# Performance work log

Measured on AMD Instinct MI355X. Metric: run time of the kernel, lower is better.

## Reference

```python
import math
import jax, jax.numpy as jnp
import numpy as np

B, S, HID = 1, 2048, 2880
H, HKV, D = 64, 8, 64
G = H // HKV  # num_key_value_groups = 8


def setup_inputs() -> dict:
    key = jax.random.key(0)
    ks = jax.random.split(key, 10)
    sd = 1.0 / math.sqrt(HID)
    hidden_states = jax.random.normal(ks[0], (B, S, HID), dtype=jnp.float32)
    # causal additive mask [B, 1, S, S]
    causal = jnp.tril(jnp.ones((S, S), dtype=bool))
    attention_mask = jnp.where(causal, 0.0, -1e9).astype(jnp.float32)[None, None]
    Wq = jax.random.normal(ks[1], (H * D, HID), dtype=jnp.float32) * sd
    bq = jax.random.normal(ks[2], (H * D,), dtype=jnp.float32) * 0.01
    Wk = jax.random.normal(ks[3], (HKV * D, HID), dtype=jnp.float32) * sd
    bk = jax.random.normal(ks[4], (HKV * D,), dtype=jnp.float32) * 0.01
    Wv = jax.random.normal(ks[5], (HKV * D, HID), dtype=jnp.float32) * sd
    bv = jax.random.normal(ks[6], (HKV * D,), dtype=jnp.float32) * 0.01
    Wo = jax.random.normal(ks[7], (HID, H * D), dtype=jnp.float32) * (1.0 / math.sqrt(H * D))
    bo = jax.random.normal(ks[8], (HID,), dtype=jnp.float32) * 0.01
    return {"hidden_states": hidden_states, "attention_mask": attention_mask,
            "Wq": Wq, "bq": bq, "Wk": Wk, "bk": bk, "Wv": Wv, "bv": bv,
            "Wo": Wo, "bo": bo}


def reference(hidden_states, attention_mask, Wq, bq, Wk, bk, Wv, bv, Wo, bo):
    b, s, _ = hidden_states.shape
    # projections
    q = hidden_states @ Wq.T + bq  # [b, s, H*D]
    k = hidden_states @ Wk.T + bk  # [b, s, HKV*D]
    v = hidden_states @ Wv.T + bv
    # torch q head index h maps to kv head h // G, so split H -> (HKV, G)
    q = q.reshape(b, s, HKV, G, D).transpose(0, 2, 3, 1, 4)   # [b, kv, g, s, d]
    k = k.reshape(b, s, HKV, D).transpose(0, 2, 1, 3)         # [b, kv, s, d]
    v = v.reshape(b, s, HKV, D).transpose(0, 2, 1, 3)
    # grouped-query attention without materializing repeated KV (same math as repeat_interleave)
    scores = jnp.einsum('bkgsd,bktd->bkgst', q, k) / math.sqrt(D)
    scores = scores + attention_mask[:, :, None]              # broadcast [b,1,1,s,t]
    attn = jax.nn.softmax(scores.astype(jnp.float32), axis=-1).astype(q.dtype)
    out = jnp.einsum('bkgst,bktd->bkgsd', attn, v)            # [b, kv, g, s, d]
    out = out.transpose(0, 3, 1, 2, 4).reshape(b, s, H * D)
    return out @ Wo.T + bo
```

## Files before the change

kernel.cpp:

```cpp
#include <hip/hip_runtime.h>
#include <hip/hip_bf16.h>
#include <cmath>

typedef __hip_bfloat16 bf16;
typedef __bf16 bf16x8 __attribute__((ext_vector_type(8)));
typedef float floatx4 __attribute__((ext_vector_type(4)));

__device__ inline floatx4 mfma16(bf16x8 a, bf16x8 b, floatx4 c) {
  return __builtin_amdgcn_mfma_f32_16x16x32_bf16(a, b, c, 0, 0, 0);
}

__device__ inline void async_ld16(const void* g, void* l) {
  __builtin_amdgcn_global_load_lds((const __attribute__((address_space(1))) void*)g,
                                   (__attribute__((address_space(3))) void*)l,
                                   16, 0, 0);
}

__device__ inline uint4 pack8(float4 a, float4 b) {
  union { uint4 u; bf16 h[8]; } t;
  t.h[0] = __float2bfloat16(a.x); t.h[1] = __float2bfloat16(a.y);
  t.h[2] = __float2bfloat16(a.z); t.h[3] = __float2bfloat16(a.w);
  t.h[4] = __float2bfloat16(b.x); t.h[5] = __float2bfloat16(b.y);
  t.h[6] = __float2bfloat16(b.z); t.h[7] = __float2bfloat16(b.w);
  return t.u;
}

__device__ inline void cvt_region(const float* __restrict__ s, bf16* __restrict__ d, int i) {
  const float4 a = ((const float4*)s)[2 * i];
  const float4 b = ((const float4*)s)[2 * i + 1];
  ((uint4*)d)[i] = pack8(a, b);
}

__global__ __launch_bounds__(256)
void cvt_all(const float* __restrict__ X,  const float* __restrict__ Wq,
             const float* __restrict__ Wk, const float* __restrict__ Wv,
             const float* __restrict__ Wo, bf16* __restrict__ Xb,
             bf16* __restrict__ Wall, bf16* __restrict__ Wob) {
  const int blk = blockIdx.x;
  const int tid = threadIdx.x;
  if (blk < 2880) {
    cvt_region(X, Xb, blk * 256 + tid);
  } else if (blk < 8640) {
    cvt_region(Wq, Wall, (blk - 2880) * 256 + tid);
  } else if (blk < 9360) {
    cvt_region(Wk, Wall + (size_t)4096 * 2880, (blk - 8640) * 256 + tid);
  } else if (blk < 10080) {
    cvt_region(Wv, Wall + (size_t)4608 * 2880, (blk - 9360) * 256 + tid);
  } else {
    cvt_region(Wo, Wob, (blk - 10080) * 256 + tid);
  }
}

#define QSCALE 0.1803368801111601f

template <int OUT_MODE>
__global__ __launch_bounds__(256)
void gemm_bt_db(const bf16* __restrict__ A, const bf16* __restrict__ B,
                const float* __restrict__ b0, const float* __restrict__ b1,
                const float* __restrict__ b2, void* __restrict__ Cp,
                void* __restrict__ Cqp, void* __restrict__ Ctp,
                int M, int N, int K, float qmul) {
  __shared__ __align__(16) bf16 sA[2][128 * 32];
  __shared__ __align__(16) bf16 sB[2][128 * 32];
  const int tid  = threadIdx.x;
  const int wave = tid >> 6;
  const int lane = tid & 63;
  const int quad = lane >> 4;
  const int l15  = lane & 15;

  const int nwg = gridDim.x * gridDim.y;
  const int lin = blockIdx.y * gridDim.x + blockIdx.x;
  const int L   = (lin & 7) * (nwg >> 3) + (lin >> 3);
  const int bm  = (L / gridDim.x) * 128;
  const int bn  = (L % gridDim.x) * 128;

  const int wm = (wave & 1) * 64;
  const int wn = (wave >> 1) * 64;

  floatx4 acc[4][4] = {};

  const int g0 = tid, g1 = tid + 256;
  const int arow0 = bm + (g0 >> 2), acol0 = (g0 & 3) * 8;
  const int arow1 = bm + (g1 >> 2), acol1 = (g1 & 3) * 8;
  int brow0 = bn + (g0 >> 2); if (brow0 >= N) brow0 = N - 1;
  int brow1 = bn + (g1 >> 2); if (brow1 >= N) brow1 = N - 1;

  const int nk = K >> 5;
  async_ld16(A + (size_t)arow0 * K + acol0, &sA[0][wave * 512]);
  async_ld16(A + (size_t)arow1 * K + acol1, &sA[0][2048 + wave * 512]);
  async_ld16(B + (size_t)brow0 * K + acol0, &sB[0][wave * 512]);
  async_ld16(B + (size_t)brow1 * K + acol1, &sB[0][2048 + wave * 512]);

  for (int kt = 0; kt < nk; ++kt) {
    __syncthreads();
    if (kt + 1 < nk) {
      const int k0 = (kt + 1) << 5;
      const int nb = (kt + 1) & 1;
      async_ld16(A + (size_t)arow0 * K + k0 + acol0, &sA[nb][wave * 512]);
      async_ld16(A + (size_t)arow1 * K + k0 + acol1, &sA[nb][2048 + wave * 512]);
      async_ld16(B + (size_t)brow0 * K + k0 + acol0, &sB[nb][wave * 512]);
      async_ld16(B + (size_t)brow1 * K + k0 + acol1, &sB[nb][2048 + wave * 512]);
    }
    const bf16* a = sA[kt & 1];
    const bf16* b = sB[kt & 1];

    bf16x8 aF[4], bF[4];
#pragma unroll
    for (int mi = 0; mi < 4; ++mi)
      aF[mi] = *(const bf16x8*)(a + (wm + mi * 16 + l15) * 32 + quad * 8);
#pragma unroll
    for (int ni = 0; ni < 4; ++ni)
      bF[ni] = *(const bf16x8*)(b + (wn + ni * 16 + l15) * 32 + quad * 8);
#pragma unroll
    for (int mi = 0; mi < 4; ++mi)
#pragma unroll
      for (int ni = 0; ni < 4; ++ni)
        acc[mi][ni] = mfma16(aF[mi], bF[ni], acc[mi][ni]);
  }

#pragma unroll
  for (int ni = 0; ni < 4; ++ni) {
    const int col = bn + wn + ni * 16 + l15;
    if (col >= N) continue;
    float bv;
    if (OUT_MODE == 4)
      bv = (col < 4096) ? b0[col] : (col < 4608 ? b1[col - 4096] : b2[col - 4608]);
    else
      bv = b0[col];
#pragma unroll
    for (int mi = 0; mi < 4; ++mi) {
      const int row = bm + wm + mi * 16 + quad * 4;
#pragma unroll
      for (int r = 0; r < 4; ++r) {
        const float val = acc[mi][ni][r] + bv;
        if (OUT_MODE == 1) {
          ((float*)Cp)[(size_t)(row + r) * N + col] = val;
        } else {
          if (col < 4096)      ((bf16*)Cp)[(size_t)(row + r) * 4096 + col] = __float2bfloat16(val * qmul);
          else if (col < 4608) ((bf16*)Cqp)[(size_t)(row + r) * 512 + (col - 4096)] = __float2bfloat16(val);
          else                 ((bf16*)Ctp)[(size_t)(col - 4608) * M + row + r] = __float2bfloat16(val);
        }
      }
    }
  }
}

template <int A_BF, int B_BF, int OUT_MODE>
__global__ __launch_bounds__(256)
void gemm_bt_bias(const void* __restrict__ Ap, const void* __restrict__ Bp,
                  const float* __restrict__ bias, void* __restrict__ Cp,
                  void* __restrict__ Cqp, void* __restrict__ Ctp,
                  int M, int N, int K, float qmul) {
  __shared__ __align__(16) bf16 sA[128 * 32];
  __shared__ __align__(16) bf16 sB[128 * 32];
  const int tid  = threadIdx.x;
  const int wave = tid >> 6;
  const int lane = tid & 63;
  const int quad = lane >> 4;
  const int l15  = lane & 15;
  const int bm = blockIdx.y * 128;
  const int bn = blockIdx.x * 128;
  const int wm = (wave & 1) * 64;
  const int wn = (wave >> 1) * 64;

  floatx4 acc[4][4] = {};

  const int g0 = tid, g1 = tid + 256;
  const int arow0 = bm + (g0 >> 2), acol0 = (g0 & 3) * 8;
  const int arow1 = bm + (g1 >> 2), acol1 = (g1 & 3) * 8;
  int brow0 = bn + (g0 >> 2); if (brow0 >= N) brow0 = N - 1;
  int brow1 = bn + (g1 >> 2); if (brow1 >= N) brow1 = N - 1;

  for (int k0 = 0; k0 < K; k0 += 32) {
    __syncthreads();
    if (A_BF) {
      const bf16* A = (const bf16*)Ap;
      async_ld16(A + (size_t)arow0 * K + k0 + acol0, sA + wave * 512);
      async_ld16(A + (size_t)arow1 * K + k0 + acol1, sA + 2048 + wave * 512);
    } else {
      const float* A = (const float*)Ap;
      const float* p0 = A + (size_t)arow0 * K + k0 + acol0;
      const float* p1 = A + (size_t)arow1 * K + k0 + acol1;
      *(uint4*)(sA + tid * 8)        = pack8(*(const float4*)p0, *(const float4*)(p0 + 4));
      *(uint4*)(sA + 2048 + tid * 8) = pack8(*(const float4*)p1, *(const float4*)(p1 + 4));
    }
    if (B_BF) {
      const bf16* B = (const bf16*)Bp;
      async_ld16(B + (size_t)brow0 * K + k0 + acol0, sB + wave * 512);
      async_ld16(B + (size_t)brow1 * K + k0 + acol1, sB + 2048 + wave * 512);
    } else {
      const float* B = (const float*)Bp;
      const float* p0 = B + (size_t)brow0 * K + k0 + acol0;
      const float* p1 = B + (size_t)brow1 * K + k0 + acol1;
      *(uint4*)(sB + tid * 8)        = pack8(*(const float4*)p0, *(const float4*)(p0 + 4));
      *(uint4*)(sB + 2048 + tid * 8) = pack8(*(const float4*)p1, *(const float4*)(p1 + 4));
    }
    __syncthreads();

    bf16x8 aF[4], bF[4];
#pragma unroll
    for (int mi = 0; mi < 4; ++mi)
      aF[mi] = *(const bf16x8*)(sA + (wm + mi * 16 + l15) * 32 + quad * 8);
#pragma unroll
    for (int ni = 0; ni < 4; ++ni)
      bF[ni] = *(const bf16x8*)(sB + (wn + ni * 16 + l15) * 32 + quad * 8);
#pragma unroll
    for (int mi = 0; mi < 4; ++mi)
#pragma unroll
      for (int ni = 0; ni < 4; ++ni)
        acc[mi][ni] = mfma16(aF[mi], bF[ni], acc[mi][ni]);
  }

#pragma unroll
  for (int ni = 0; ni < 4; ++ni) {
    const int col = bn + wn + ni * 16 + l15;
    if (col >= N) continue;
    const float bv = bias[col];
#pragma unroll
    for (int mi = 0; mi < 4; ++mi) {
      const int row = bm + wm + mi * 16 + quad * 4;
#pragma unroll
      for (int r = 0; r < 4; ++r) {
        const float val = acc[mi][ni][r] + bv;
        if (OUT_MODE == 0) {
          ((bf16*)Cp)[(size_t)(row + r) * N + col] = __float2bfloat16(val * qmul);
        } else if (OUT_MODE == 1) {
          ((float*)Cp)[(size_t)(row + r) * N + col] = val;
        } else if (OUT_MODE == 2) {
          ((bf16*)Ctp)[(size_t)col * M + row + r] = __float2bfloat16(val);
        }
      }
    }
  }
}

__global__ __launch_bounds__(256)
void attn_fused(const bf16* __restrict__ Q, const bf16* __restrict__ Kc,
                const bf16* __restrict__ Vt, bf16* __restrict__ AO) {
  constexpr int HD = 4096, KD = 512, SEQ = 2048;
  constexpr float NEG = -1e30f;
  __shared__ __align__(16) bf16 sP[64 * 64];
  __shared__ __align__(16) bf16 sK[2][64 * 64];
  __shared__ __align__(16) bf16 sV[2][64 * 64];

  const int lin = blockIdx.y * 32 + blockIdx.x;
  const int L   = (lin & 7) * 256 + (lin >> 3);
  const int h   = L >> 5;
  const int qb  = 31 - (L & 31);
  const int kvh = h >> 3;
  const int tid = threadIdx.x, wave = tid >> 6, lane = tid & 63;
  const int quad = lane >> 4, l15 = lane & 15;
  const int sq0 = qb * 64;

  const int lrow = lane >> 3;
  const int lgr  = (lane & 7) ^ lrow;

  bf16x8 qf[2];
#pragma unroll
  for (int ks = 0; ks < 2; ++ks)
    qf[ks] = *(const bf16x8*)(Q + (size_t)(sq0 + wave * 16 + l15) * HD + h * 64 + ks * 32 + quad * 8);

  bf16x8 onesf;
#pragma unroll
  for (int i = 0; i < 8; ++i) onesf[i] = (__bf16)1.0f;

#pragma unroll
  for (int i = 0; i < 2; ++i) {
    const int c = wave * 2 + i;
    async_ld16(Kc + (size_t)(c * 8 + lrow) * KD + kvh * 64 + lgr * 8, &sK[0][c * 512]);
    async_ld16(Vt + (size_t)(kvh * 64 + c * 8 + lrow) * SEQ + lgr * 8, &sV[0][c * 512]);
  }

  floatx4 o_acc[4] = {};
  floatx4 o_sum = {};
  float m_run = NEG;

  for (int kt = 0; kt <= qb; ++kt) {
    const int st0 = kt * 64;
    __syncthreads();

    if (kt < qb) {
      const int st1 = st0 + 64;
      const int nb = (kt + 1) & 1;
#pragma unroll
      for (int i = 0; i < 2; ++i) {
        const int c = wave * 2 + i;
        async_ld16(Kc + (size_t)(st1 + c * 8 + lrow) * KD + kvh * 64 + lgr * 8, &sK[nb][c * 512]);
        async_ld16(Vt + (size_t)(kvh * 64 + c * 8 + lrow) * SEQ + st1 + lgr * 8, &sV[nb][c * 512]);
      }
    }
    const bf16* kb = sK[kt & 1];
    const bf16* vb = sV[kt & 1];

    floatx4 s_acc[4] = {};
#pragma unroll
    for (int ks = 0; ks < 2; ++ks) {
#pragma unroll
      for (int ni = 0; ni < 4; ++ni) {
        const bf16x8 kF = *(const bf16x8*)(kb + (ni * 16 + l15) * 64 + (((ks * 4 + quad) ^ (l15 & 7)) * 8));
        s_acc[ni] = mfma16(kF, qf[ks], s_acc[ni]);
      }
    }

    if (kt == qb) {
      const int qloc = wave * 16 + l15;
#pragma unroll
      for (int ni = 0; ni < 4; ++ni)
#pragma unroll
        for (int r = 0; r < 4; ++r)
          if (ni * 16 + quad * 4 + r > qloc) s_acc[ni][r] = NEG;
    }

    float t0 = fmaxf(fmaxf(s_acc[0][0], s_acc[0][1]), fmaxf(s_acc[0][2], s_acc[0][3]));
    float t1 = fmaxf(fmaxf(s_acc[1][0], s_acc[1][1]), fmaxf(s_acc[1][2], s_acc[1][3]));
    float t2 = fmaxf(fmaxf(s_acc[2][0], s_acc[2][1]), fmaxf(s_acc[2][2], s_acc[2][3]));
    float t3 = fmaxf(fmaxf(s_acc[3][0], s_acc[3][1]), fmaxf(s_acc[3][2], s_acc[3][3]));
    float tm = fmaxf(fmaxf(t0, t1), fmaxf(t2, t3));
    tm = fmaxf(tm, __shfl_xor(tm, 16));
    tm = fmaxf(tm, __shfl_xor(tm, 32));

    if (!__all(tm - m_run <= 8.0f)) {
      const float mn = fmaxf(m_run, tm);
      const float alpha = exp2f(m_run - mn);
      m_run = mn;
#pragma unroll
      for (int r = 0; r < 4; ++r) o_sum[r] *= alpha;
#pragma unroll
      for (int di = 0; di < 4; ++di)
#pragma unroll
        for (int r = 0; r < 4; ++r) o_acc[di][r] *= alpha;
    }

    const int prow = wave * 16 + l15;
#pragma unroll
    for (int ni = 0; ni < 4; ++ni) {
      union { uint2 u; bf16 hh[4]; } pk;
#pragma unroll
      for (int r = 0; r < 4; ++r)
        pk.hh[r] = __float2bfloat16(exp2f(s_acc[ni][r] - m_run));
      const int g = ni * 2 + (quad >> 1);
      *(uint2*)(sP + prow * 64 + ((g ^ (l15 & 7)) * 8) + (quad & 1) * 4) = pk.u;
    }

#pragma unroll
    for (int ks = 0; ks < 2; ++ks) {
      const bf16x8 pF = *(const bf16x8*)(sP + prow * 64 + (((ks * 4 + quad) ^ (l15 & 7)) * 8));
#pragma unroll
      for (int di = 0; di < 4; ++di) {
        const bf16x8 vF = *(const bf16x8*)(vb + (di * 16 + l15) * 64 + (((ks * 4 + quad) ^ (l15 & 7)) * 8));
        o_acc[di] = mfma16(vF, pF, o_acc[di]);
      }
      o_sum = mfma16(onesf, pF, o_sum);
    }
  }

  const float inv = 1.0f / o_sum[0];
  const int row = sq0 + wave * 16 + l15;
#pragma unroll
  for (int di = 0; di < 4; ++di) {
    union { uint2 u; bf16 hh[4]; } pk;
#pragma unroll
    for (int r = 0; r < 4; ++r)
      pk.hh[r] = __float2bfloat16(o_acc[di][r] * inv);
    *(uint2*)(AO + (size_t)row * HD + h * 64 + di * 16 + quad * 4) = pk.u;
  }
}

extern "C" void kernel_launch(void* const* d_in, const int* in_sizes, int n_in,
                              void* d_out, int out_size, void* d_ws, size_t ws_size,
                              hipStream_t stream) {
  const float* X  = (const float*)d_in[0];
  const float* Wq = (const float*)d_in[2];
  const float* bq = (const float*)d_in[3];
  const float* Wk = (const float*)d_in[4];
  const float* bk = (const float*)d_in[5];
  const float* Wv = (const float*)d_in[6];
  const float* bv = (const float*)d_in[7];
  const float* Wo = (const float*)d_in[8];
  const float* bo = (const float*)d_in[9];
  float* out = (float*)d_out;

  char* ws = (char*)d_ws;
  bf16* Qb = (bf16*)(ws);
  bf16* Kb = (bf16*)(ws + 16777216);
  bf16* Vt = (bf16*)(ws + 18874368);
  bf16* AO = (bf16*)(ws + 20971520);
  bf16*  Xb   = (bf16*)(ws + 37748736);
  bf16*  Wall = (bf16*)(ws + 49545216);
  bf16*  Wob  = (bf16*)(ws + 79036416);
  const size_t NEED = 102629376;

  dim3 blk(256);
  if (ws_size >= NEED) {
    cvt_all<<<dim3(15840), blk, 0, stream>>>(X, Wq, Wk, Wv, Wo, Xb, Wall, Wob);

    gemm_bt_db<4><<<dim3(40, 16), blk, 0, stream>>>(Xb, Wall, bq, bk, bv, Qb, Kb, Vt, 2048, 5120, 2880, QSCALE);
    attn_fused<<<dim3(32, 64), blk, 0, stream>>>(Qb, Kb, Vt, AO);
    gemm_bt_db<1><<<dim3(23, 16), blk, 0, stream>>>(AO, Wob, bo, nullptr, nullptr, out, nullptr, nullptr, 2048, 2880, 4096, 1.f);
  } else {
    gemm_bt_bias<0, 0, 0><<<dim3(32, 16), blk, 0, stream>>>(X, Wq, bq, Qb, nullptr, nullptr, 2048, 4096, 2880, QSCALE);
    gemm_bt_bias<0, 0, 0><<<dim3(4, 16),  blk, 0, stream>>>(X, Wk, bk, Kb, nullptr, nullptr, 2048, 512, 2880, 1.f);
    gemm_bt_bias<0, 0, 2><<<dim3(4, 16),  blk, 0, stream>>>(X, Wv, bv, nullptr, nullptr, Vt, 2048, 512, 2880, 1.f);
    attn_fused<<<dim3(32, 64), blk, 0, stream>>>(Qb, Kb, Vt, AO);
    gemm_bt_bias<1, 0, 1><<<dim3(23, 16), blk, 0, stream>>>(AO, Wo, bo, out, nullptr, nullptr, 2048, 2880, 4096, 1.f);
  }
}
```

Measured before the change: 444.7 us.

## Process 128 query rows per attention block with 8 waves sharing K/V tiles

The attention kernel now uses 512-thread blocks covering 128 query rows (two 64-row subtiles), halving the grid. Each K/V tile loaded into LDS is reused by twice as many waves, and each wave issues one async load per tile instead of two, cutting global K/V traffic. Waves in the lower subtile skip compute for the final tile via a continue but still join the barriers, which adds some idle time and raises LDS and register pressure per block. The continue placement depends on the hidden loop tail containing no barrier.

```diff
diff --git a/kernel.cpp b/kernel.cpp
--- a/kernel.cpp
+++ b/kernel.cpp
@@ -234,23 +234,25 @@
   }
 }
 
-__global__ __launch_bounds__(256)
+__global__ __launch_bounds__(512)
 void attn_fused(const bf16* __restrict__ Q, const bf16* __restrict__ Kc,
                 const bf16* __restrict__ Vt, bf16* __restrict__ AO) {
   constexpr int HD = 4096, KD = 512, SEQ = 2048;
   constexpr float NEG = -1e30f;
-  __shared__ __align__(16) bf16 sP[64 * 64];
+  __shared__ __align__(16) bf16 sP[128 * 64];
   __shared__ __align__(16) bf16 sK[2][64 * 64];
   __shared__ __align__(16) bf16 sV[2][64 * 64];
 
-  const int lin = blockIdx.y * 32 + blockIdx.x;
-  const int L   = (lin & 7) * 256 + (lin >> 3);
-  const int h   = L >> 5;
-  const int qb  = 31 - (L & 31);
+  const int lin = blockIdx.y * 16 + blockIdx.x;
+  const int L   = (lin & 7) * 128 + (lin >> 3);
+  const int h   = L >> 4;
+  const int sb  = 15 - (L & 15);
   const int kvh = h >> 3;
   const int tid = threadIdx.x, wave = tid >> 6, lane = tid & 63;
   const int quad = lane >> 4, l15 = lane & 15;
-  const int sq0 = qb * 64;
+  const int sq0 = sb * 128;
+  const int qbw = 2 * sb + (wave >> 2);
+  const int qbm = 2 * sb + 1;
 
   const int lrow = lane >> 3;
   const int lgr  = (lane & 7) ^ lrow;
@@ -264,31 +266,25 @@
 #pragma unroll
   for (int i = 0; i < 8; ++i) onesf[i] = (__bf16)1.0f;
 
-#pragma unroll
-  for (int i = 0; i < 2; ++i) {
-    const int c = wave * 2 + i;
-    async_ld16(Kc + (size_t)(c * 8 + lrow) * KD + kvh * 64 + lgr * 8, &sK[0][c * 512]);
-    async_ld16(Vt + (size_t)(kvh * 64 + c * 8 + lrow) * SEQ + lgr * 8, &sV[0][c * 512]);
-  }
+  async_ld16(Kc + (size_t)(wave * 8 + lrow) * KD + kvh * 64 + lgr * 8, &sK[0][wave * 512]);
+  async_ld16(Vt + (size_t)(kvh * 64 + wave * 8 + lrow) * SEQ + lgr * 8, &sV[0][wave * 512]);
 
   floatx4 o_acc[4] = {};
   floatx4 o_sum = {};
   float m_run = NEG;
 
-  for (int kt = 0; kt <= qb; ++kt) {
+  for (int kt = 0; kt <= qbm; ++kt) {
     const int st0 = kt * 64;
     __syncthreads();
 
-    if (kt < qb) {
+    if (kt < qbm) {
       const int st1 = st0 + 64;
       const int nb = (kt + 1) & 1;
-#pragma unroll
-      for (int i = 0; i < 2; ++i) {
-        const int c = wave * 2 + i;
-        async_ld16(Kc + (size_t)(st1 + c * 8 + lrow) * KD + kvh * 64 + lgr * 8, &sK[nb][c * 512]);
-        async_ld16(Vt + (size_t)(kvh * 64 + c * 8 + lrow) * SEQ + st1 + lgr * 8, &sV[nb][c * 512]);
-      }
-    }
+      async_ld16(Kc + (size_t)(st1 + wave * 8 + lrow) * KD + kvh * 64 + lgr * 8, &sK[nb][wave * 512]);
+      async_ld16(Vt + (size_t)(kvh * 64 + wave * 8 + lrow) * SEQ + st1 + lgr * 8, &sV[nb][wave * 512]);
+    }
+    if (kt > qbw) continue;
+
     const bf16* kb = sK[kt & 1];
     const bf16* vb = sV[kt & 1];
 
@@ -302,8 +298,8 @@
       }
     }
 
-    if (kt == qb) {
-      const int qloc = wave * 16 + l15;
+    if (kt == qbw) {
+      const int qloc = (wave & 3) * 16 + l15;
 #pragma unroll
       for (int ni = 0; ni < 4; ++ni)
 #pragma unroll
@@ -395,13 +391,13 @@
     cvt_all<<<dim3(15840), blk, 0, stream>>>(X, Wq, Wk, Wv, Wo, Xb, Wall, Wob);
 
     gemm_bt_db<4><<<dim3(40, 16), blk, 0, stream>>>(Xb, Wall, bq, bk, bv, Qb, Kb, Vt, 2048, 5120, 2880, QSCALE);
-    attn_fused<<<dim3(32, 64), blk, 0, stream>>>(Qb, Kb, Vt, AO);
+    attn_fused<<<dim3(16, 64), dim3(512), 0, stream>>>(Qb, Kb, Vt, AO);
     gemm_bt_db<1><<<dim3(23, 16), blk, 0, stream>>>(AO, Wob, bo, nullptr, nullptr, out, nullptr, nullptr, 2048, 2880, 4096, 1.f);
   } else {
     gemm_bt_bias<0, 0, 0><<<dim3(32, 16), blk, 0, stream>>>(X, Wq, bq, Qb, nullptr, nullptr, 2048, 4096, 2880, QSCALE);
     gemm_bt_bias<0, 0, 0><<<dim3(4, 16),  blk, 0, stream>>>(X, Wk, bk, Kb, nullptr, nullptr, 2048, 512, 2880, 1.f);
     gemm_bt_bias<0, 0, 2><<<dim3(4, 16),  blk, 0, stream>>>(X, Wv, bv, nullptr, nullptr, Vt, 2048, 512, 2880, 1.f);
-    attn_fused<<<dim3(32, 64), blk, 0, stream>>>(Qb, Kb, Vt, AO);
+    attn_fused<<<dim3(16, 64), dim3(512), 0, stream>>>(Qb, Kb, Vt, AO);
     gemm_bt_bias<1, 0, 1><<<dim3(23, 16), blk, 0, stream>>>(AO, Wo, bo, out, nullptr, nullptr, 2048, 2880, 4096, 1.f);
   }
 }
```

New measurement: 454.2 us. +2.1%, slower.
